# Performance work log

Measured on AMD Instinct MI355X. Metric: run time of the kernel, lower is better.

## Reference

```python
import jax, jax.numpy as jnp
import numpy as np

N_TOKEN = 8192
N_EMBED = 512
DECAY = 0.99
EPS = 1e-08


def setup_inputs() -> dict:
    key = jax.random.key(0)
    k1, k2, k3, k4 = jax.random.split(key, 4)
    inputs = jax.random.normal(k1, (4, 4096, N_EMBED), dtype=jnp.float32)
    key_w = jax.random.normal(k2, (N_TOKEN, N_EMBED), dtype=jnp.float32)
    value_w = jax.random.normal(k3, (N_TOKEN, N_EMBED), dtype=jnp.float32)
    ema_n = jnp.ones((N_TOKEN,), dtype=jnp.float32)
    ema_w = jax.random.normal(k4, (N_TOKEN, N_EMBED), dtype=jnp.float32)
    return {"inputs": inputs, "key_w": key_w, "value_w": value_w,
            "ema_n": ema_n, "ema_w": ema_w}


def reference(inputs, key_w, value_w, ema_n, ema_w):
    size = inputs.shape
    x = inputs.reshape(-1, N_EMBED)  # [T, D]

    # squared euclidean distances to key codebook: [T, n_token]
    dists = (jnp.sum(x * x, axis=-1, keepdims=True)
             + jnp.sum(key_w * key_w, axis=-1)[None, :]
             - 2.0 * jnp.matmul(x, key_w.T))
    indices = jnp.argmin(dists, axis=-1)  # [T] int

    quantized = (x + value_w[indices]).reshape(size)

    # --- training-mode EMA codebook update (torch .data ops, no grad) ---
    T = x.shape[0]
    ratio = float(N_TOKEN) / T
    # cnts[k] = ratio * (#tokens assigned to k)
    cnts = jnp.zeros((N_TOKEN,), dtype=x.dtype).at[indices].add(ratio)
    # ws = one_hot(indices).T @ x scaled by ratio  (segment sum over codes)
    ws = jax.ops.segment_sum(x, indices, num_segments=N_TOKEN) * ratio
    ema_n_new = ema_n * DECAY + (1.0 - DECAY) * cnts
    ema_w_new = ema_w * DECAY + (1.0 - DECAY) * ws
    # renormalize keys (Laplace-smoothed counts)
    n = jnp.sum(ema_n_new)
    sz = (ema_n_new + EPS) / (n + EPS * N_TOKEN) * n
    key_w_new = ema_w_new / sz[:, None]

    return quantized, ema_n_new, ema_w_new, key_w_new
```

## Files before the change

### kernel.cpp

```cpp
#include <hip/hip_runtime.h>

#define N_TOKEN 8192
#define N_EMBED 512
#define T_TOKENS 16384
#define KP 1536
#define KPM 1024
#define MARGIN 0.45f
#define NBG 8

typedef __bf16 bf16x8 __attribute__((ext_vector_type(8)));
typedef __bf16 bf16x4 __attribute__((ext_vector_type(4)));
typedef float f32x4 __attribute__((ext_vector_type(4)));

__device__ __forceinline__ unsigned int fkey(float f) {
  unsigned int u = __float_as_uint(f);
  return (u & 0x80000000u) ? ~u : (u | 0x80000000u);
}
__device__ __forceinline__ void gl2lds16(const void* gsrc, void* lds) {
  __builtin_amdgcn_global_load_lds(
      (const __attribute__((address_space(1))) unsigned int*)gsrc,
      (__attribute__((address_space(3))) unsigned int*)lds, 16, 0, 0);
}
__device__ __forceinline__ unsigned long long umin64(unsigned long long a,
                                                     unsigned long long b) {
  return a < b ? a : b;
}

__device__ __forceinline__ void pack_hl_body(const float* __restrict__ src,
                                             __bf16* __restrict__ dstbuf, int gid) {
  int t = gid >> 7, d4 = gid & 127;
  float4 v = reinterpret_cast<const float4*>(src)[gid];
  bf16x4 hi, lo;
  hi[0] = (__bf16)v.x; hi[1] = (__bf16)v.y; hi[2] = (__bf16)v.z; hi[3] = (__bf16)v.w;
  lo[0] = (__bf16)(v.x - (float)hi[0]);
  lo[1] = (__bf16)(v.y - (float)hi[1]);
  lo[2] = (__bf16)(v.z - (float)hi[2]);
  lo[3] = (__bf16)(v.w - (float)hi[3]);
  __bf16* row = dstbuf + (size_t)t * KPM + d4 * 4;
  *(bf16x4*)(row)       = hi;
  *(bf16x4*)(row + 512) = lo;
}

__device__ __forceinline__ void pack_k_body(const float* __restrict__ kw,
                                            __bf16* __restrict__ kp,
                                            float* __restrict__ h,
                                            int blk, int tid) {
  int row = blk * 4 + (tid >> 6);
  int lane = tid & 63;
  const float4* src = reinterpret_cast<const float4*>(kw + (size_t)row * N_EMBED);
  __bf16* dst = kp + (size_t)row * KPM;
  float s = 0.f;
  #pragma unroll
  for (int c = 0; c < 2; ++c) {
    int f4 = lane + c * 64;
    float4 v = src[f4];
    s += v.x*v.x + v.y*v.y + v.z*v.z + v.w*v.w;
    bf16x4 hi, lo;
    hi[0] = (__bf16)v.x; hi[1] = (__bf16)v.y; hi[2] = (__bf16)v.z; hi[3] = (__bf16)v.w;
    lo[0] = (__bf16)(v.x - (float)hi[0]);
    lo[1] = (__bf16)(v.y - (float)hi[1]);
    lo[2] = (__bf16)(v.z - (float)hi[2]);
    lo[3] = (__bf16)(v.w - (float)hi[3]);
    *(bf16x4*)(dst + f4 * 4)       = hi;
    *(bf16x4*)(dst + 512 + f4 * 4) = lo;
  }
  #pragma unroll
  for (int off = 32; off; off >>= 1) s += __shfl_down(s, off);
  if (lane == 0) h[row] = 0.5f * s;
}

__global__ void k_pack_all(const float* __restrict__ x, const float* __restrict__ kw,
                           const float* __restrict__ ema_n,
                           __bf16* __restrict__ xp, __bf16* __restrict__ kp,
                           float* __restrict__ h, float* __restrict__ nsum,
                           unsigned int* __restrict__ ucount, int* __restrict__ counts) {
  int b = blockIdx.x;
  if (b < 8192) {
    pack_hl_body(x, xp, b * 256 + threadIdx.x);
  } else if (b < 10240) {
    pack_k_body(kw, kp, h, b - 8192, threadIdx.x);
  } else if (b == 10240) {
    __shared__ float sm[256];
    float s = 0.f;
    for (int i = threadIdx.x; i < N_TOKEN; i += 256) s += ema_n[i];
    sm[threadIdx.x] = s;
    __syncthreads();
    for (int off = 128; off; off >>= 1) {
      if (threadIdx.x < off) sm[threadIdx.x] += sm[threadIdx.x + off];
      __syncthreads();
    }
    if (threadIdx.x == 0) { *nsum = sm[0]; *ucount = 0u; }
  } else {
    for (int i = threadIdx.x; i < N_TOKEN; i += 256) counts[i] = 0;
  }
}

__global__ void k_pack_x(const float* __restrict__ x, __bf16* __restrict__ xp) {
  pack_hl_body(x, xp, blockIdx.x * blockDim.x + threadIdx.x);
}
__global__ void k_pack_k_norm(const float* __restrict__ kw, __bf16* __restrict__ kp,
                              float* __restrict__ h) {
  pack_k_body(kw, kp, h, blockIdx.x, threadIdx.x);
}

__global__ void k_hnorm(const float* __restrict__ key_w, float* __restrict__ h) {
  int code = blockIdx.x * 4 + (threadIdx.x >> 6);
  int lane = threadIdx.x & 63;
  const float4* row = reinterpret_cast<const float4*>(key_w + (size_t)code * N_EMBED);
  float s = 0.f;
  float4 v0 = row[lane];
  float4 v1 = row[lane + 64];
  s += v0.x*v0.x + v0.y*v0.y + v0.z*v0.z + v0.w*v0.w;
  s += v1.x*v1.x + v1.y*v1.y + v1.z*v1.z + v1.w*v1.w;
  #pragma unroll
  for (int off = 32; off; off >>= 1) s += __shfl_down(s, off);
  if (lane == 0) h[code] = 0.5f * s;
}

#define BMr 128
#define BNr 128
#define BKe 64

__global__ __launch_bounds__(256, 2) void k_mfma_top2(
    const __bf16* __restrict__ xp, const __bf16* __restrict__ kp,
    const float* __restrict__ h, float4* __restrict__ slots) {
  __shared__ __bf16 AS[128 * 128];
  __shared__ __bf16 BS[128 * 128];

  const int b = blockIdx.x;
  const int xcd = b & 7, chunk = b >> 3;
  const int mb = xcd * 16 + (chunk & 15);
  const int nbg = chunk >> 4;
  const int m0 = mb * BMr;
  const int tid = threadIdx.x;
  const int lane = tid & 63;
  const int wid = tid >> 6;
  const int wm = wid * 32;
  const int soff = tid * 16;
  const int rgrp = lane >> 4;
  const int cidx = lane & 15;

  float rs1[8], rs2[8];
  int rc1[8];
  #pragma unroll
  for (int u = 0; u < 8; ++u) { rs1[u] = 3.4e38f; rs2[u] = 3.4e38f; rc1[u] = 0; }

  for (int q = 0; q < NBG; ++q) {
    const int n0 = (nbg * NBG + q) * BNr;
    f32x4 acc[2][8] = {};

    for (int ks = 0; ks < 512; ks += 128) {
      __syncthreads();
      #pragma unroll
      for (int i = 0; i < 8; ++i) {
        int off = i * 4096 + soff;
        int row = off >> 8;
        int inner = (off & 255) ^ ((row & 7) << 4);
        gl2lds16(xp + (size_t)(m0 + row) * KPM + ks + (inner >> 1), (char*)AS + off);
        gl2lds16(kp + (size_t)(n0 + row) * KPM + ks + (inner >> 1), (char*)BS + off);
      }
      asm volatile("s_waitcnt vmcnt(0)" ::: "memory");
      __syncthreads();

      #pragma unroll
      for (int kk = 0; kk < 4; ++kk) {
        const int cbyte = kk * 64 + (lane >> 4) * 16;
        bf16x8 af[2], bb[8];
        #pragma unroll
        for (int i = 0; i < 2; ++i) {
          int arow = wm + i * 16 + (lane & 15);
          af[i] = *(const bf16x8*)((const char*)AS + arow * 256 + (cbyte ^ ((arow & 7) << 4)));
        }
        #pragma unroll
        for (int j = 0; j < 8; ++j) {
          int brow = j * 16 + (lane & 15);
          bb[j] = *(const bf16x8*)((const char*)BS + brow * 256 + (cbyte ^ ((brow & 7) << 4)));
        }
        #pragma unroll
        for (int i = 0; i < 2; ++i)
          #pragma unroll
          for (int j = 0; j < 8; ++j)
            acc[i][j] = __builtin_amdgcn_mfma_f32_16x16x32_bf16(af[i], bb[j], acc[i][j], 0, 0, 0);
      }
    }

    #pragma unroll
    for (int i = 0; i < 2; ++i) {
      #pragma unroll
      for (int r = 0; r < 4; ++r) {
        const int u = i * 4 + r;
        float s1 = rs1[u], s2 = rs2[u];
        int c1 = rc1[u];
        #pragma unroll
        for (int j = 0; j < 8; ++j) {
          int kk = n0 + j * 16 + cidx;
          float sc = h[kk] - acc[i][j][r];
          if (sc < s1) { s2 = s1; s1 = sc; c1 = kk; }
          else s2 = fminf(s2, sc);
        }
        rs1[u] = s1; rs2[u] = s2; rc1[u] = c1;
      }
    }
  }

  #pragma unroll
  for (int u = 0; u < 8; ++u) {
    float s1 = rs1[u], s2 = rs2[u];
    int c1 = rc1[u];
    #pragma unroll
    for (int msk = 1; msk < 16; msk <<= 1) {
      float o1 = __shfl_xor(s1, msk);
      float o2 = __shfl_xor(s2, msk);
      int   oc = __shfl_xor(c1, msk);
      float ns2 = fminf(fminf(s2, o2), fmaxf(s1, o1));
      bool take = o1 < s1;
      s1 = take ? o1 : s1;
      c1 = take ? oc : c1;
      s2 = ns2;
    }
    if (cidx == 0) {
      int row = m0 + wm + (u >> 2) * 16 + rgrp * 4 + (u & 3);
      float4 p;
      p.x = s1; p.y = s2; p.z = __int_as_float(c1); p.w = 0.f;
      slots[(size_t)row * NBG + nbg] = p;
    }
  }
}

__global__ void k_top2_reduce(const float4* __restrict__ slots,
                              int* __restrict__ idx, unsigned int* __restrict__ tlist,
                              unsigned int* __restrict__ ucount,
                              int* __restrict__ counts,
                              unsigned long long* __restrict__ rbest) {
  int tid = threadIdx.x;
  int lane = tid & 63, wid = tid >> 6;
  int row = blockIdx.x * 32 + wid * 8 + (lane >> 3);
  int slot = lane & 7;
  float4 a = slots[(size_t)row * NBG + slot];
  float s1 = a.x, s2 = a.y;
  int c1 = __float_as_int(a.z);
  #pragma unroll
  for (int msk = 1; msk < 8; msk <<= 1) {
    float o1 = __shfl_xor(s1, msk);
    float o2 = __shfl_xor(s2, msk);
    int   oc = __shfl_xor(c1, msk);
    float ns2 = fminf(fminf(s2, o2), fmaxf(s1, o1));
    bool take = o1 < s1;
    s1 = take ? o1 : s1;
    c1 = take ? oc : c1;
    s2 = ns2;
  }
  if (slot == 0) {
    if (s2 - s1 >= MARGIN) {
      idx[row] = c1;
      atomicAdd(&counts[c1], 1);
    } else {
      unsigned int p = atomicAdd(ucount, 1u);
      tlist[p] = (unsigned int)row;
      rbest[p] = ~0ull;
    }
  }
}

__global__ __launch_bounds__(256) void k_mfma_refine(
    const __bf16* __restrict__ xp, const __bf16* __restrict__ kp,
    const float* __restrict__ h, const unsigned int* __restrict__ tlist,
    const unsigned int* __restrict__ ucount, unsigned long long* __restrict__ rbest) {
  const unsigned int uc = *ucount;
  const int nb = blockIdx.x, mb = blockIdx.y;
  const int m0 = mb * BMr;
  if ((unsigned int)m0 >= uc) return;

  __shared__ __bf16 AS[BMr * BKe];
  __shared__ __bf16 BS[BNr * BKe];

  const int n0 = nb * BNr;
  const int tid = threadIdx.x;
  const int lane = tid & 63;
  const int wid = tid >> 6;
  const int wm = (wid >> 1) * 64, wn = (wid & 1) * 64;

  const int r0 = tid >> 3;
  size_t abase[4];
  #pragma unroll
  for (int i = 0; i < 4; ++i) {
    int p = m0 + r0 + 32 * i;
    int pc = p < (int)uc ? p : (int)uc - 1;
    abase[i] = (size_t)tlist[pc] * KPM;
  }

  f32x4 acc[4][4] = {};
  const int soff = tid * 16;
  const int innerC = (soff & 127) ^ ((r0 & 7) << 4);

  for (int ks = 0; ks < KP; ks += BKe) {
    const int ksA = ks < 512 ? ks : ks - 512;
    const int ksB = ks < 1024 ? ks : ks - 1024;
    __syncthreads();
    #pragma unroll
    for (int i = 0; i < 4; ++i) {
      int off = i * 4096 + soff;
      int brow = (off >> 7);
      gl2lds16(xp + abase[i] + ksA + (innerC >> 1), (char*)AS + off);
      int binner = (off & 127) ^ ((brow & 7) << 4);
      gl2lds16(kp + (size_t)(n0 + brow) * KPM + ksB + (binner >> 1), (char*)BS + off);
    }
    asm volatile("s_waitcnt vmcnt(0)" ::: "memory");
    __syncthreads();

    #pragma unroll
    for (int kk = 0; kk < 2; ++kk) {
      const int cbyte = kk * 64 + (lane >> 4) * 16;
      bf16x8 af[4], bb[4];
      #pragma unroll
      for (int i = 0; i < 4; ++i) {
        int arow = wm + i * 16 + (lane & 15);
        af[i] = *(const bf16x8*)((const char*)AS + arow * 128 + (cbyte ^ ((arow & 7) << 4)));
        int brow = wn + i * 16 + (lane & 15);
        bb[i] = *(const bf16x8*)((const char*)BS + brow * 128 + (cbyte ^ ((brow & 7) << 4)));
      }
      #pragma unroll
      for (int i = 0; i < 4; ++i)
        #pragma unroll
        for (int j = 0; j < 4; ++j)
          acc[i][j] = __builtin_amdgcn_mfma_f32_16x16x32_bf16(af[i], bb[j], acc[i][j], 0, 0, 0);
    }
  }

  const int rgrp = lane >> 4;
  const int cidx = lane & 15;
  #pragma unroll
  for (int i = 0; i < 4; ++i) {
    #pragma unroll
    for (int r = 0; r < 4; ++r) {
      unsigned long long m = ~0ull;
      #pragma unroll
      for (int j = 0; j < 4; ++j) {
        int kk = n0 + wn + j * 16 + cidx;
        float score = h[kk] - acc[i][j][r];
        unsigned long long cand =
            ((unsigned long long)fkey(score) << 32) | (unsigned int)kk;
        m = umin64(m, cand);
      }
      #pragma unroll
      for (int msk = 1; msk < 16; msk <<= 1) m = umin64(m, __shfl_xor(m, msk));
      if (cidx == 0) {
        int p = m0 + wm + i * 16 + rgrp * 4 + r;
        if ((unsigned int)p < uc) atomicMin(&rbest[p], m);
      }
    }
  }
}

__global__ void k_finalize(const unsigned long long* __restrict__ rbest,
                           const unsigned int* __restrict__ tlist,
                           const unsigned int* __restrict__ ucount,
                           int* __restrict__ idx, int* __restrict__ counts) {
  unsigned int p = blockIdx.x * 256 + threadIdx.x;
  if (p < *ucount) {
    int k = (int)(unsigned int)(rbest[p] & 0xffffffffull);
    idx[tlist[p]] = k;
    atomicAdd(&counts[k], 1);
  }
}

__global__ void k_scan(const int* __restrict__ counts, int* __restrict__ offs,
                       int* __restrict__ cursor) {
  __shared__ int sa[256], sb[256];
  int tid = threadIdx.x;
  int base = tid * 32;
  int loc[32]; int s = 0;
  #pragma unroll
  for (int e = 0; e < 32; ++e) { loc[e] = s; s += counts[base + e]; }
  sa[tid] = s;
  __syncthreads();
  int* src = sa; int* dst = sb;
  for (int d = 1; d < 256; d <<= 1) {
    int v = src[tid] + (tid >= d ? src[tid - d] : 0);
    dst[tid] = v;
    __syncthreads();
    int* tmp = src; src = dst; dst = tmp;
  }
  int excl = src[tid] - s;
  #pragma unroll
  for (int e = 0; e < 32; ++e) {
    int o = excl + loc[e];
    offs[base + e] = o;
    cursor[base + e] = o;
  }
}

__global__ void k_place(const int* __restrict__ idx, int* __restrict__ cursor,
                        int* __restrict__ tok) {
  int t = blockIdx.x * 256 + threadIdx.x;
  if (t < T_TOKENS) {
    int p = atomicAdd(&cursor[idx[t]], 1);
    tok[p] = t;
  }
}

__global__ void k_update(const float* __restrict__ x, const float* __restrict__ ema_n,
                         const float* __restrict__ ema_w, const float* __restrict__ value_w,
                         const int* __restrict__ counts,
                         const int* __restrict__ offs, const int* __restrict__ tok,
                         const float* __restrict__ nsum,
                         float* __restrict__ out_en, float* __restrict__ out_ew,
                         float* __restrict__ out_kw, float* __restrict__ out_q) {
  int k = blockIdx.x * 4 + (threadIdx.x >> 6);
  int lane = threadIdx.x & 63;
  int cnt = counts[k];
  int off = offs[k];
  float en = 0.99f * ema_n[k] + 0.005f * (float)cnt;
  if (lane == 0) out_en[k] = en;
  float n = 0.99f * (*nsum) + 81.92f;
  float sz = (en + 1e-8f) / (n + 1e-8f * (float)N_TOKEN) * n;

  const float4* er = reinterpret_cast<const float4*>(ema_w + (size_t)k * N_EMBED);
  float4 e0 = er[lane], e1 = er[lane + 64];
  const float4* vr = reinterpret_cast<const float4*>(value_w + (size_t)k * N_EMBED);
  float4 v0 = vr[lane], v1 = vr[lane + 64];
  float4 s0 = {0.f, 0.f, 0.f, 0.f}, s1v = {0.f, 0.f, 0.f, 0.f};
  for (int q = 0; q < cnt; ++q) {
    int t = tok[off + q];
    const float4* xr = reinterpret_cast<const float4*>(x + (size_t)t * N_EMBED);
    float4 a = xr[lane], b = xr[lane + 64];
    s0.x += a.x; s0.y += a.y; s0.z += a.z; s0.w += a.w;
    s1v.x += b.x; s1v.y += b.y; s1v.z += b.z; s1v.w += b.w;
    float4 qa, qb;
    qa.x = a.x + v0.x; qa.y = a.y + v0.y; qa.z = a.z + v0.z; qa.w = a.w + v0.w;
    qb.x = b.x + v1.x; qb.y = b.y + v1.y; qb.z = b.z + v1.z; qb.w = b.w + v1.w;
    float4* oq = reinterpret_cast<float4*>(out_q + (size_t)t * N_EMBED);
    oq[lane] = qa; oq[lane + 64] = qb;
  }
  float4 w0, w1;
  w0.x = 0.99f * e0.x + 0.005f * s0.x;  w0.y = 0.99f * e0.y + 0.005f * s0.y;
  w0.z = 0.99f * e0.z + 0.005f * s0.z;  w0.w = 0.99f * e0.w + 0.005f * s0.w;
  w1.x = 0.99f * e1.x + 0.005f * s1v.x; w1.y = 0.99f * e1.y + 0.005f * s1v.y;
  w1.z = 0.99f * e1.z + 0.005f * s1v.z; w1.w = 0.99f * e1.w + 0.005f * s1v.w;
  float4* ow = reinterpret_cast<float4*>(out_ew + (size_t)k * N_EMBED);
  ow[lane] = w0; ow[lane + 64] = w1;
  float4 q0, q1;
  q0.x = w0.x / sz; q0.y = w0.y / sz; q0.z = w0.z / sz; q0.w = w0.w / sz;
  q1.x = w1.x / sz; q1.y = w1.y / sz; q1.z = w1.z / sz; q1.w = w1.w / sz;
  float4* okw = reinterpret_cast<float4*>(out_kw + (size_t)k * N_EMBED);
  okw[lane] = q0; okw[lane + 64] = q1;
}

__global__ void k_quant(const float* __restrict__ x, const float* __restrict__ value_w,
                        const int* __restrict__ idx, float* __restrict__ q) {
  int gid = blockIdx.x * blockDim.x + threadIdx.x;
  int t = gid >> 7, d4 = gid & 127;
  float4 xv = reinterpret_cast<const float4*>(x)[gid];
  float4 v = reinterpret_cast<const float4*>(value_w + (size_t)idx[t] * N_EMBED)[d4];
  float4 o;
  o.x = xv.x + v.x; o.y = xv.y + v.y; o.z = xv.z + v.z; o.w = xv.w + v.w;
  reinterpret_cast<float4*>(q)[gid] = o;
}

__global__ __launch_bounds__(256) void k_mfma_argmin(
    const __bf16* __restrict__ xp, const __bf16* __restrict__ kp,
    const float* __restrict__ h, unsigned long long* __restrict__ best) {
  __shared__ __bf16 AS[BMr * BKe];
  __shared__ __bf16 BS[BNr * BKe];
  const int nb = blockIdx.x, mb = blockIdx.y;
  const int m0 = mb * BMr, n0 = nb * BNr;
  const int tid = threadIdx.x;
  const int lane = tid & 63;
  const int wid = tid >> 6;
  const int wm = (wid >> 1) * 64, wn = (wid & 1) * 64;
  f32x4 acc[4][4] = {};
  const int soff = tid * 16;
  for (int ks = 0; ks < KP; ks += BKe) {
    const int ksA = ks < 512 ? ks : ks - 512;
    const int ksB = ks < 1024 ? ks : ks - 1024;
    __syncthreads();
    #pragma unroll
    for (int i = 0; i < 4; ++i) {
      int off = i * 4096 + soff;
      int row = off >> 7;
      int inner = (off & 127) ^ ((row & 7) << 4);
      gl2lds16(xp + (size_t)(m0 + row) * KPM + ksA + (inner >> 1), (char*)AS + off);
      gl2lds16(kp + (size_t)(n0 + row) * KPM + ksB + (inner >> 1), (char*)BS + off);
    }
    asm volatile("s_waitcnt vmcnt(0)" ::: "memory");
    __syncthreads();
    #pragma unroll
    for (int kk = 0; kk < 2; ++kk) {
      const int cbyte = kk * 64 + (lane >> 4) * 16;
      bf16x8 af[4], bb[4];
      #pragma unroll
      for (int i = 0; i < 4; ++i) {
        int arow = wm + i * 16 + (lane & 15);
        af[i] = *(const bf16x8*)((const char*)AS + arow * 128 + (cbyte ^ ((arow & 7) << 4)));
        int brow = wn + i * 16 + (lane & 15);
        bb[i] = *(const bf16x8*)((const char*)BS + brow * 128 + (cbyte ^ ((brow & 7) << 4)));
      }
      #pragma unroll
      for (int i = 0; i < 4; ++i)
        #pragma unroll
        for (int j = 0; j < 4; ++j)
          acc[i][j] = __builtin_amdgcn_mfma_f32_16x16x32_bf16(af[i], bb[j], acc[i][j], 0, 0, 0);
    }
  }
  const int rgrp = lane >> 4;
  const int cidx = lane & 15;
  #pragma unroll
  for (int i = 0; i < 4; ++i) {
    #pragma unroll
    for (int r = 0; r < 4; ++r) {
      unsigned long long m = ~0ull;
      #pragma unroll
      for (int j = 0; j < 4; ++j) {
        int kk = n0 + wn + j * 16 + cidx;
        float score = h[kk] - acc[i][j][r];
        unsigned long long cand =
            ((unsigned long long)fkey(score) << 32) | (unsigned int)kk;
        m = umin64(m, cand);
      }
      #pragma unroll
      for (int msk = 1; msk < 16; msk <<= 1) m = umin64(m, __shfl_xor(m, msk));
      if (cidx == 0) {
        int row = m0 + wm + i * 16 + rgrp * 4 + r;
        atomicMin(&best[row], m);
      }
    }
  }
}

#define BT 128
#define BK 128
#define DC 32
__global__ __launch_bounds__(256, 2) void k_gemm_argmin(
    const float* __restrict__ x, const float* __restrict__ key_w,
    const float* __restrict__ h, unsigned long long* __restrict__ best) {
  __shared__ float4 XS[BT * 8];
  __shared__ float4 KS[BK * 8];
  const int kb = blockIdx.x, tb = blockIdx.y;
  const int t0 = tb * BT, k0 = kb * BK;
  const int tid = threadIdx.x;
  const int tx = tid & 15;
  const int tyg = tid >> 4;
  float acc[8][8];
  #pragma unroll
  for (int i = 0; i < 8; ++i)
    #pragma unroll
    for (int j = 0; j < 8; ++j) acc[i][j] = 0.f;
  for (int dc = 0; dc < N_EMBED; dc += DC) {
    __syncthreads();
    #pragma unroll
    for (int ld = 0; ld < 4; ++ld) {
      int li = ld * 256 + tid;
      int row = li >> 3, c4 = li & 7;
      XS[row * 8 + (c4 ^ (row & 7))] =
          *reinterpret_cast<const float4*>(x + (size_t)(t0 + row) * N_EMBED + dc + c4 * 4);
      KS[row * 8 + (c4 ^ (row & 7))] =
          *reinterpret_cast<const float4*>(key_w + (size_t)(k0 + row) * N_EMBED + dc + c4 * 4);
    }
    __syncthreads();
    #pragma unroll
    for (int d4 = 0; d4 < 8; ++d4) {
      float4 a[8], b[8];
      #pragma unroll
      for (int j = 0; j < 8; ++j) {
        a[j] = XS[(tyg + 16 * j) * 8 + (d4 ^ (tyg & 7))];
        b[j] = KS[(tx  + 16 * j) * 8 + (d4 ^ (tx  & 7))];
      }
      #pragma unroll
      for (int i = 0; i < 8; ++i) {
        float4 av = a[i];
        #pragma unroll
        for (int j = 0; j < 8; ++j) {
          float4 bv = b[j];
          acc[i][j] = fmaf(av.x, bv.x, fmaf(av.y, bv.y,
                      fmaf(av.z, bv.z, fmaf(av.w, bv.w, acc[i][j]))));
        }
      }
    }
  }
  #pragma unroll
  for (int i = 0; i < 8; ++i) {
    unsigned long long m = ~0ull;
    #pragma unroll
    for (int j = 0; j < 8; ++j) {
      int kk = k0 + tx + 16 * j;
      float score = h[kk] - acc[i][j];
      unsigned long long cand =
          ((unsigned long long)fkey(score) << 32) | (unsigned int)kk;
      m = umin64(m, cand);
    }
    #pragma unroll
    for (int mask = 1; mask < 16; mask <<= 1) m = umin64(m, __shfl_xor(m, mask));
    if (tx == 0) atomicMin(&best[t0 + tyg + 16 * i], m);
  }
}

__global__ void k_extract_counts(const unsigned long long* __restrict__ best,
                                 int* __restrict__ idx, float* __restrict__ out_en) {
  int t = blockIdx.x * blockDim.x + threadIdx.x;
  if (t < T_TOKENS) {
    int k = (int)(unsigned int)(best[t] & 0xffffffffull);
    idx[t] = k;
    atomicAdd(&out_en[k], 0.005f);
  }
}
__global__ void k_quant_scatter(const float* __restrict__ x,
                                const float* __restrict__ value_w,
                                const int* __restrict__ idx,
                                float* __restrict__ q, float* __restrict__ out_ew) {
  int gid = blockIdx.x * blockDim.x + threadIdx.x;
  int t = gid >> 7, d4 = gid & 127;
  float4 xv = reinterpret_cast<const float4*>(x)[gid];
  int k = idx[t];
  float4 v = reinterpret_cast<const float4*>(value_w + (size_t)k * N_EMBED)[d4];
  float4 o;
  o.x = xv.x + v.x; o.y = xv.y + v.y; o.z = xv.z + v.z; o.w = xv.w + v.w;
  reinterpret_cast<float4*>(q)[gid] = o;
  const float c = 0.005f;
  float* dst = out_ew + (size_t)k * N_EMBED + d4 * 4;
  atomicAdd(dst + 0, c * xv.x);
  atomicAdd(dst + 1, c * xv.y);
  atomicAdd(dst + 2, c * xv.z);
  atomicAdd(dst + 3, c * xv.w);
}
__global__ void k_scaleN(const float* __restrict__ ema_n, float* __restrict__ out_en) {
  int k = blockIdx.x * blockDim.x + threadIdx.x;
  if (k < N_TOKEN) out_en[k] = 0.99f * ema_n[k];
}
__global__ void k_scaleW(const float* __restrict__ ema_w, float* __restrict__ out_ew) {
  int gid = blockIdx.x * blockDim.x + threadIdx.x;
  float4 v = reinterpret_cast<const float4*>(ema_w)[gid];
  float4 o;
  o.x = 0.99f * v.x; o.y = 0.99f * v.y; o.z = 0.99f * v.z; o.w = 0.99f * v.w;
  reinterpret_cast<float4*>(out_ew)[gid] = o;
}
__global__ void k_sumn(const float* __restrict__ en, float* __restrict__ nsum) {
  __shared__ float sm[256];
  float s = 0.f;
  for (int i = threadIdx.x; i < N_TOKEN; i += 256) s += en[i];
  sm[threadIdx.x] = s;
  __syncthreads();
  for (int off = 128; off; off >>= 1) {
    if (threadIdx.x < off) sm[threadIdx.x] += sm[threadIdx.x + off];
    __syncthreads();
  }
  if (threadIdx.x == 0) *nsum = sm[0];
}
__global__ void k_keyw(const float* __restrict__ out_ew, const float* __restrict__ out_en,
                       const float* __restrict__ nsum, float* __restrict__ out_kw) {
  int gid = blockIdx.x * blockDim.x + threadIdx.x;
  int k = gid >> 7;
  float n = *nsum;
  float sz = (out_en[k] + 1e-8f) / (n + 1e-8f * (float)N_TOKEN) * n;
  float4 w = reinterpret_cast<const float4*>(out_ew)[gid];
  float4 o;
  o.x = w.x / sz; o.y = w.y / sz; o.z = w.z / sz; o.w = w.w / sz;
  reinterpret_cast<float4*>(out_kw)[gid] = o;
}

extern "C" void kernel_launch(void* const* d_in, const int* in_sizes, int n_in,
                              void* d_out, int out_size, void* d_ws, size_t ws_size,
                              hipStream_t stream) {
  const float* x       = (const float*)d_in[0];
  const float* key_w   = (const float*)d_in[1];
  const float* value_w = (const float*)d_in[2];
  const float* ema_n   = (const float*)d_in[3];
  const float* ema_w   = (const float*)d_in[4];

  float* out_q  = (float*)d_out;
  float* out_en = out_q + 8388608;
  float* out_ew = out_en + N_TOKEN;
  float* out_kw = out_ew + 4194304;

  const size_t SLOTS_B = (size_t)T_TOKENS * NBG * 16;
  const size_t XP_B    = (size_t)T_TOKENS * KPM * 2;
  const size_t KP_B    = (size_t)N_TOKEN * KPM * 2;
  char* base = (char*)d_ws;
  float4* slots = (float4*)base;
  __bf16* xp2 = (__bf16*)(base + SLOTS_B);
  __bf16* kp2 = (__bf16*)(base + SLOTS_B + XP_B);
  char* tail  = base + SLOTS_B + XP_B + KP_B;
  float* h                  = (float*)(tail + 0);
  int*   idx                = (int*)(tail + 32768);
  unsigned int* tlist       = (unsigned int*)(tail + 98304);
  unsigned long long* rbest = (unsigned long long*)(tail + 163840);
  unsigned int* ucount      = (unsigned int*)(tail + 294912);
  float* nsum               = (float*)(tail + 295168);
  int* counts               = (int*)(tail + 295424);
  int* offs                 = (int*)(tail + 328192);
  int* cursor               = (int*)(tail + 360960);
  int* tok                  = (int*)(tail + 393728);
  const size_t ws_need2 = SLOTS_B + XP_B + KP_B + 459264;

  unsigned long long* f_best = (unsigned long long*)d_ws;
  int*   f_idx  = (int*)((char*)d_ws + 131072);
  float* f_h    = (float*)((char*)d_ws + 196608);
  float* f_nsum = (float*)((char*)d_ws + 229376);
  __bf16* f_xp  = (__bf16*)((char*)d_ws + 262144);
  __bf16* f_kp  = (__bf16*)((char*)d_ws + 262144 + XP_B);
  const size_t ws_need1 = 262144 + XP_B + KP_B;

  if (ws_size >= ws_need2) {
    k_pack_all<<<10242, 256, 0, stream>>>(x, key_w, ema_n, xp2, kp2, h, nsum,
                                          ucount, counts);
    k_mfma_top2<<<1024, 256, 0, stream>>>(xp2, kp2, h, slots);
    k_top2_reduce<<<T_TOKENS / 32, 256, 0, stream>>>(slots, idx, tlist, ucount,
                                                     counts, rbest);
    {
      dim3 grid(N_TOKEN / BNr, T_TOKENS / BMr);
      k_mfma_refine<<<grid, 256, 0, stream>>>(xp2, kp2, h, tlist, ucount, rbest);
    }
    k_finalize<<<T_TOKENS / 256, 256, 0, stream>>>(rbest, tlist, ucount, idx, counts);

    k_scan<<<1, 256, 0, stream>>>(counts, offs, cursor);
    k_place<<<T_TOKENS / 256, 256, 0, stream>>>(idx, cursor, tok);
    k_update<<<N_TOKEN / 4, 256, 0, stream>>>(x, ema_n, ema_w, value_w, counts,
                                              offs, tok, nsum,
                                              out_en, out_ew, out_kw, out_q);
  } else if (ws_size >= ws_need1) {
    hipMemsetAsync(f_best, 0xFF, (size_t)T_TOKENS * 8, stream);
    k_pack_x<<<(T_TOKENS * (N_EMBED / 4)) / 256, 256, 0, stream>>>(x, f_xp);
    k_pack_k_norm<<<N_TOKEN / 4, 256, 0, stream>>>(key_w, f_kp, f_h);
    dim3 grid(N_TOKEN / BNr, T_TOKENS / BMr);
    k_mfma_argmin<<<grid, 256, 0, stream>>>(f_xp, f_kp, f_h, f_best);

    k_scaleN<<<N_TOKEN / 256, 256, 0, stream>>>(ema_n, out_en);
    k_extract_counts<<<T_TOKENS / 256, 256, 0, stream>>>(f_best, f_idx, out_en);
    k_scaleW<<<(N_TOKEN * (N_EMBED / 4)) / 256, 256, 0, stream>>>(ema_w, out_ew);
    k_quant_scatter<<<(T_TOKENS * (N_EMBED / 4)) / 256, 256, 0, stream>>>(
        x, value_w, f_idx, out_q, out_ew);
    k_sumn<<<1, 256, 0, stream>>>(out_en, f_nsum);
    k_keyw<<<(N_TOKEN * (N_EMBED / 4)) / 256, 256, 0, stream>>>(out_ew, out_en, f_nsum, out_kw);
  } else {
    hipMemsetAsync(f_best, 0xFF, (size_t)T_TOKENS * 8, stream);
    k_hnorm<<<N_TOKEN / 4, 256, 0, stream>>>(key_w, f_h);
    dim3 grid(N_TOKEN / BK, T_TOKENS / BT);
    k_gemm_argmin<<<grid, 256, 0, stream>>>(x, key_w, f_h, f_best);

    k_scaleN<<<N_TOKEN / 256, 256, 0, stream>>>(ema_n, out_en);
    k_extract_counts<<<T_TOKENS / 256, 256, 0, stream>>>(f_best, f_idx, out_en);
    k_scaleW<<<(N_TOKEN * (N_EMBED / 4)) / 256, 256, 0, stream>>>(ema_w, out_ew);
    k_quant_scatter<<<(T_TOKENS * (N_EMBED / 4)) / 256, 256, 0, stream>>>(
        x, value_w, f_idx, out_q, out_ew);
    k_sumn<<<1, 256, 0, stream>>>(out_en, f_nsum);
    k_keyw<<<(N_TOKEN * (N_EMBED / 4)) / 256, 256, 0, stream>>>(out_ew, out_en, f_nsum, out_kw);
  }
}
```

Measured before the change: 356.3 us.

## Rebalance top2 grid, vectorize x packing, and grid-stride the refine kernel

```diff
diff --git a/kernel.cpp b/kernel.cpp
--- a/kernel.cpp
+++ b/kernel.cpp
@@ -6,7 +6,8 @@
 #define KP 1536
 #define KPM 1024
 #define MARGIN 0.45f
-#define NBG 8
+#define NBG 16
+#define NSLOT 4
 
 typedef __bf16 bf16x8 __attribute__((ext_vector_type(8)));
 typedef __bf16 bf16x4 __attribute__((ext_vector_type(4)));
@@ -41,6 +42,28 @@
   *(bf16x4*)(row + 512) = lo;
 }
 
+__device__ __forceinline__ void pack_hl_body2(const float* __restrict__ src,
+                                              __bf16* __restrict__ dstbuf, int gid) {
+  int f0 = gid * 2;
+  int t = f0 >> 7, d4 = f0 & 127;
+  float4 v0 = reinterpret_cast<const float4*>(src)[f0];
+  float4 v1 = reinterpret_cast<const float4*>(src)[f0 + 1];
+  bf16x8 hi, lo;
+  hi[0] = (__bf16)v0.x; hi[1] = (__bf16)v0.y; hi[2] = (__bf16)v0.z; hi[3] = (__bf16)v0.w;
+  hi[4] = (__bf16)v1.x; hi[5] = (__bf16)v1.y; hi[6] = (__bf16)v1.z; hi[7] = (__bf16)v1.w;
+  lo[0] = (__bf16)(v0.x - (float)hi[0]);
+  lo[1] = (__bf16)(v0.y - (float)hi[1]);
+  lo[2] = (__bf16)(v0.z - (float)hi[2]);
+  lo[3] = (__bf16)(v0.w - (float)hi[3]);
+  lo[4] = (__bf16)(v1.x - (float)hi[4]);
+  lo[5] = (__bf16)(v1.y - (float)hi[5]);
+  lo[6] = (__bf16)(v1.z - (float)hi[6]);
+  lo[7] = (__bf16)(v1.w - (float)hi[7]);
+  __bf16* row = dstbuf + (size_t)t * KPM + d4 * 4;
+  *(bf16x8*)(row)       = hi;
+  *(bf16x8*)(row + 512) = lo;
+}
+
 __device__ __forceinline__ void pack_k_body(const float* __restrict__ kw,
                                             __bf16* __restrict__ kp,
                                             float* __restrict__ h,
@@ -75,11 +98,11 @@
                            float* __restrict__ h, float* __restrict__ nsum,
                            unsigned int* __restrict__ ucount, int* __restrict__ counts) {
   int b = blockIdx.x;
-  if (b < 8192) {
-    pack_hl_body(x, xp, b * 256 + threadIdx.x);
-  } else if (b < 10240) {
-    pack_k_body(kw, kp, h, b - 8192, threadIdx.x);
-  } else if (b == 10240) {
+  if (b < 4096) {
+    pack_hl_body2(x, xp, b * 256 + threadIdx.x);
+  } else if (b < 6144) {
+    pack_k_body(kw, kp, h, b - 4096, threadIdx.x);
+  } else if (b == 6144) {
     __shared__ float sm[256];
     float s = 0.f;
     for (int i = threadIdx.x; i < N_TOKEN; i += 256) s += ema_n[i];
@@ -222,7 +245,7 @@
       int row = m0 + wm + (u >> 2) * 16 + rgrp * 4 + (u & 3);
       float4 p;
       p.x = s1; p.y = s2; p.z = __int_as_float(c1); p.w = 0.f;
-      slots[(size_t)row * NBG + nbg] = p;
+      slots[(size_t)row * NSLOT + nbg] = p;
     }
   }
 }
@@ -234,13 +257,13 @@
                               unsigned long long* __restrict__ rbest) {
   int tid = threadIdx.x;
   int lane = tid & 63, wid = tid >> 6;
-  int row = blockIdx.x * 32 + wid * 8 + (lane >> 3);
-  int slot = lane & 7;
-  float4 a = slots[(size_t)row * NBG + slot];
+  int row = blockIdx.x * 64 + wid * 16 + (lane >> 2);
+  int slot = lane & 3;
+  float4 a = slots[(size_t)row * NSLOT + slot];
   float s1 = a.x, s2 = a.y;
   int c1 = __float_as_int(a.z);
   #pragma unroll
-  for (int msk = 1; msk < 8; msk <<= 1) {
+  for (int msk = 1; msk < 4; msk <<= 1) {
     float o1 = __shfl_xor(s1, msk);
     float o2 = __shfl_xor(s2, msk);
     int   oc = __shfl_xor(c1, msk);
@@ -267,88 +290,88 @@
     const float* __restrict__ h, const unsigned int* __restrict__ tlist,
     const unsigned int* __restrict__ ucount, unsigned long long* __restrict__ rbest) {
   const unsigned int uc = *ucount;
-  const int nb = blockIdx.x, mb = blockIdx.y;
-  const int m0 = mb * BMr;
-  if ((unsigned int)m0 >= uc) return;
-
-  __shared__ __bf16 AS[BMr * BKe];
-  __shared__ __bf16 BS[BNr * BKe];
-
+  const int nb = blockIdx.x;
   const int n0 = nb * BNr;
   const int tid = threadIdx.x;
   const int lane = tid & 63;
   const int wid = tid >> 6;
   const int wm = (wid >> 1) * 64, wn = (wid & 1) * 64;
-
   const int r0 = tid >> 3;
-  size_t abase[4];
-  #pragma unroll
-  for (int i = 0; i < 4; ++i) {
-    int p = m0 + r0 + 32 * i;
-    int pc = p < (int)uc ? p : (int)uc - 1;
-    abase[i] = (size_t)tlist[pc] * KPM;
-  }
-
-  f32x4 acc[4][4] = {};
   const int soff = tid * 16;
   const int innerC = (soff & 127) ^ ((r0 & 7) << 4);
-
-  for (int ks = 0; ks < KP; ks += BKe) {
-    const int ksA = ks < 512 ? ks : ks - 512;
-    const int ksB = ks < 1024 ? ks : ks - 1024;
-    __syncthreads();
-    #pragma unroll
-    for (int i = 0; i < 4; ++i) {
-      int off = i * 4096 + soff;
-      int brow = (off >> 7);
-      gl2lds16(xp + abase[i] + ksA + (innerC >> 1), (char*)AS + off);
-      int binner = (off & 127) ^ ((brow & 7) << 4);
-      gl2lds16(kp + (size_t)(n0 + brow) * KPM + ksB + (binner >> 1), (char*)BS + off);
-    }
-    asm volatile("s_waitcnt vmcnt(0)" ::: "memory");
-    __syncthreads();
-
-    #pragma unroll
-    for (int kk = 0; kk < 2; ++kk) {
-      const int cbyte = kk * 64 + (lane >> 4) * 16;
-      bf16x8 af[4], bb[4];
-      #pragma unroll
-      for (int i = 0; i < 4; ++i) {
-        int arow = wm + i * 16 + (lane & 15);
-        af[i] = *(const bf16x8*)((const char*)AS + arow * 128 + (cbyte ^ ((arow & 7) << 4)));
-        int brow = wn + i * 16 + (lane & 15);
-        bb[i] = *(const bf16x8*)((const char*)BS + brow * 128 + (cbyte ^ ((brow & 7) << 4)));
-      }
-      #pragma unroll
-      for (int i = 0; i < 4; ++i)
-        #pragma unroll
-        for (int j = 0; j < 4; ++j)
-          acc[i][j] = __builtin_amdgcn_mfma_f32_16x16x32_bf16(af[i], bb[j], acc[i][j], 0, 0, 0);
-    }
-  }
-
   const int rgrp = lane >> 4;
   const int cidx = lane & 15;
-  #pragma unroll
-  for (int i = 0; i < 4; ++i) {
-    #pragma unroll
-    for (int r = 0; r < 4; ++r) {
-      unsigned long long m = ~0ull;
-      #pragma unroll
-      for (int j = 0; j < 4; ++j) {
-        int kk = n0 + wn + j * 16 + cidx;
-        float score = h[kk] - acc[i][j][r];
-        unsigned long long cand =
-            ((unsigned long long)fkey(score) << 32) | (unsigned int)kk;
-        m = umin64(m, cand);
-      }
-      #pragma unroll
-      for (int msk = 1; msk < 16; msk <<= 1) m = umin64(m, __shfl_xor(m, msk));
-      if (cidx == 0) {
-        int p = m0 + wm + i * 16 + rgrp * 4 + r;
-        if ((unsigned int)p < uc) atomicMin(&rbest[p], m);
-      }
-    }
+
+  __shared__ __bf16 AS[BMr * BKe];
+  __shared__ __bf16 BS[BNr * BKe];
+
+  for (int mb = blockIdx.y; mb * BMr < (int)uc; mb += 16) {
+    const int m0 = mb * BMr;
+    size_t abase[4];
+    #pragma unroll
+    for (int i = 0; i < 4; ++i) {
+      int p = m0 + r0 + 32 * i;
+      int pc = p < (int)uc ? p : (int)uc - 1;
+      abase[i] = (size_t)tlist[pc] * KPM;
+    }
+
+    f32x4 acc[4][4] = {};
+    for (int ks = 0; ks < KP; ks += BKe) {
+      const int ksA = ks < 512 ? ks : ks - 512;
+      const int ksB = ks < 1024 ? ks : ks - 1024;
+      __syncthreads();
+      #pragma unroll
+      for (int i = 0; i < 4; ++i) {
+        int off = i * 4096 + soff;
+        int brow = (off >> 7);
+        gl2lds16(xp + abase[i] + ksA + (innerC >> 1), (char*)AS + off);
+        int binner = (off & 127) ^ ((brow & 7) << 4);
+        gl2lds16(kp + (size_t)(n0 + brow) * KPM + ksB + (binner >> 1), (char*)BS + off);
+      }
+      asm volatile("s_waitcnt vmcnt(0)" ::: "memory");
+      __syncthreads();
+
+      #pragma unroll
+      for (int kk = 0; kk < 2; ++kk) {
+        const int cbyte = kk * 64 + (lane >> 4) * 16;
+        bf16x8 af[4], bb[4];
+        #pragma unroll
+        for (int i = 0; i < 4; ++i) {
+          int arow = wm + i * 16 + (lane & 15);
+          af[i] = *(const bf16x8*)((const char*)AS + arow * 128 + (cbyte ^ ((arow & 7) << 4)));
+          int brow = wn + i * 16 + (lane & 15);
+          bb[i] = *(const bf16x8*)((const char*)BS + brow * 128 + (cbyte ^ ((brow & 7) << 4)));
+        }
+        #pragma unroll
+        for (int i = 0; i < 4; ++i)
+          #pragma unroll
+          for (int j = 0; j < 4; ++j)
+            acc[i][j] = __builtin_amdgcn_mfma_f32_16x16x32_bf16(af[i], bb[j], acc[i][j], 0, 0, 0);
+      }
+    }
+
+    #pragma unroll
+    for (int i = 0; i < 4; ++i) {
+      #pragma unroll
+      for (int r = 0; r < 4; ++r) {
+        unsigned long long m = ~0ull;
+        #pragma unroll
+        for (int j = 0; j < 4; ++j) {
+          int kk = n0 + wn + j * 16 + cidx;
+          float score = h[kk] - acc[i][j][r];
+          unsigned long long cand =
+              ((unsigned long long)fkey(score) << 32) | (unsigned int)kk;
+          m = umin64(m, cand);
+        }
+        #pragma unroll
+        for (int msk = 1; msk < 16; msk <<= 1) m = umin64(m, __shfl_xor(m, msk));
+        if (cidx == 0) {
+          int p = m0 + wm + i * 16 + rgrp * 4 + r;
+          if ((unsigned int)p < uc) atomicMin(&rbest[p], m);
+        }
+      }
+    }
+    __syncthreads();
   }
 }
 
@@ -671,7 +694,7 @@
   float* out_ew = out_en + N_TOKEN;
   float* out_kw = out_ew + 4194304;
 
-  const size_t SLOTS_B = (size_t)T_TOKENS * NBG * 16;
+  const size_t SLOTS_B = (size_t)T_TOKENS * NSLOT * 16;
   const size_t XP_B    = (size_t)T_TOKENS * KPM * 2;
   const size_t KP_B    = (size_t)N_TOKEN * KPM * 2;
   char* base = (char*)d_ws;
@@ -700,13 +723,13 @@
   const size_t ws_need1 = 262144 + XP_B + KP_B;
 
   if (ws_size >= ws_need2) {
-    k_pack_all<<<10242, 256, 0, stream>>>(x, key_w, ema_n, xp2, kp2, h, nsum,
-                                          ucount, counts);
-    k_mfma_top2<<<1024, 256, 0, stream>>>(xp2, kp2, h, slots);
-    k_top2_reduce<<<T_TOKENS / 32, 256, 0, stream>>>(slots, idx, tlist, ucount,
+    k_pack_all<<<6146, 256, 0, stream>>>(x, key_w, ema_n, xp2, kp2, h, nsum,
+                                         ucount, counts);
+    k_mfma_top2<<<512, 256, 0, stream>>>(xp2, kp2, h, slots);
+    k_top2_reduce<<<T_TOKENS / 64, 256, 0, stream>>>(slots, idx, tlist, ucount,
                                                      counts, rbest);
     {
-      dim3 grid(N_TOKEN / BNr, T_TOKENS / BMr);
+      dim3 grid(N_TOKEN / BNr, 16);
       k_mfma_refine<<<grid, 256, 0, stream>>>(xp2, kp2, h, tlist, ucount, rbest);
     }
     k_finalize<<<T_TOKENS / 256, 256, 0, stream>>>(rbest, tlist, ucount, idx, counts);
```

After: 368.5 us. 1.03x slower.
